# Optimization experiments

Measured on AMD Instinct MI355X. Metric: run time of the kernel, lower is better.

## Reference

```python
import jax, jax.numpy as jnp
import numpy as np

B, T, E, H = 16, 4096, 64, 8
K, GADD, RADD, REGION = 256, 8, 8, 64
MIN_SIGMA, SIGMA_SCALE, SIGMA_BOOST = 0.05, 1.0, 2.0
VS = K * (4 + GADD + RADD)


def setup_inputs() -> dict:
    key = jax.random.key(0)
    ks = jax.random.split(key, 10)
    return {
        "x": jax.random.normal(ks[0], (B, T, E), jnp.float32),
        "Wq": jax.random.normal(ks[1], (E, E * H), jnp.float32) / np.float32(np.sqrt(E)),
        "Wk": jax.random.normal(ks[2], (E, E * H), jnp.float32) / np.float32(np.sqrt(E)),
        "Wv": jax.random.normal(ks[3], (E, E * H), jnp.float32) / np.float32(np.sqrt(E)),
        "Wu": jax.random.normal(ks[4], (H * E, E), jnp.float32) / np.float32(np.sqrt(H * E)),
        "bu": jnp.zeros((E,), jnp.float32),
        "means_p": jax.random.normal(ks[5], (K, 2), jnp.float32),
        "sigmas_p": jax.random.normal(ks[6], (K,), jnp.float32),
        "global_ints": jax.random.randint(ks[7], (B, 1, K, GADD, 2), 0, T, jnp.int32),
        "local_offsets": jax.random.randint(ks[8], (B, 1, K, RADD, 2), 0, REGION, jnp.int32),
    }


def _flip(x):
    # util.flip: sort each (i, j) pair so row >= col (below-diagonal / causal)
    hi = jnp.max(x, axis=-1, keepdims=True)
    lo = jnp.min(x, axis=-1, keepdims=True)
    return jnp.concatenate([hi, lo], axis=-1)


def _forward(x, Wq, Wk, Wv, Wu, bu, means_p, sigmas_p, global_ints, local_offsets):
    b, t, e = x.shape
    h, k = H, K

    # ---- hyper(): continuous means/sigmas over the (t, t) attention matrix
    means = jnp.broadcast_to(means_p[None, None], (b, 1, k, 2))
    means = _flip(means)
    means = jax.nn.sigmoid(means) * (t - 1)                       # (b,1,k,2) in [0, t-1]
    sig = jax.nn.softplus(sigmas_p + SIGMA_BOOST) + MIN_SIGMA     # (k,)
    sigmas = jnp.broadcast_to((sig * t * SIGMA_SCALE)[None, None, :, None], (b, 1, k, 2))

    # ---- ngenerate: 2^rank floor/ceil neighbours + global + relative-window samples
    fl, ce = jnp.floor(means), jnp.ceil(means)
    pat = jnp.array([[0., 0.], [0., 1.], [1., 0.], [1., 1.]], jnp.float32)  # (4,2)
    neigh = fl[:, :, :, None, :] * (1.0 - pat) + ce[:, :, :, None, :] * pat
    neigh = jnp.clip(neigh, 0, t - 1).astype(jnp.int32)           # (b,1,k,4,2)
    lower = jnp.clip(jnp.floor(means) - REGION // 2, 0, t - REGION).astype(jnp.int32)
    local = lower[:, :, :, None, :] + local_offsets               # (b,1,k,RADD,2)
    idx = jnp.concatenate([neigh, global_ints, local], axis=3).reshape(b, 1, VS, 2)
    idx = _flip(idx)                                              # (b,1,VS,2), row >= col

    # ---- densities: unnormalized Gaussian weight of each int tuple under each point
    indfl = idx.astype(jnp.float32)
    diff = (indfl[:, :, :, None, :] - means[:, :, None, :, :]) / sigmas[:, :, None, :, :]
    props = jnp.exp(-0.5 * jnp.sum(diff * diff, axis=-1))         # (b,1,VS,K)

    # ---- nduplicates: zero all-but-one of identical index tuples per batch
    ids = idx[:, 0, :, 0] * t + idx[:, 0, :, 1]                   # (b, VS)
    def dupmask(v):
        o = jnp.argsort(v)
        s = v[o]
        d = jnp.concatenate([jnp.zeros((1,), bool), s[1:] == s[:-1]])
        return jnp.zeros((VS,), bool).at[o].set(d)
    dups = jax.vmap(dupmask)(ids)                                  # (b, VS)
    props = jnp.where(dups[:, None, :, None], 0.0, props)
    props = props / jnp.sum(props, axis=2, keepdims=True)
    weights = jnp.sum(props, axis=3)                               # mvalues == 1 -> (b,1,VS)

    # ---- Q/K/V projections, per-head dim = e
    scale = e ** -0.25
    q = (x @ Wq).reshape(b, t, h, e).transpose(0, 2, 1, 3).reshape(b * h, t, e) * scale
    kk = (x @ Wk).reshape(b, t, h, e).transpose(0, 2, 1, 3).reshape(b * h, t, e) * scale
    v = (x @ Wv).reshape(b, t, h, e).transpose(0, 2, 1, 3).reshape(b * h, t, e)

    rows = jnp.broadcast_to(idx[:, 0, None, :, 0], (b, h, VS)).reshape(b * h, VS)
    cols = jnp.broadcast_to(idx[:, 0, None, :, 1], (b, h, VS)).reshape(b * h, VS)
    w = jnp.broadcast_to(weights[:, 0, None, :], (b, h, VS)).reshape(b * h, VS)

    sq = jnp.take_along_axis(q, rows[:, :, None], axis=1)          # (b*h, VS, e)
    sk = jnp.take_along_axis(kk, cols[:, :, None], axis=1)
    dot = w * jnp.sum(sq * sk, axis=-1)                            # (b*h, VS)

    # ---- segment (row-wise) softmax over the sparse pattern
    seg = (jnp.arange(b * h, dtype=jnp.int32)[:, None] * t + rows).reshape(-1)
    dflat = dot.reshape(-1)
    m = jax.lax.stop_gradient(jax.ops.segment_max(dflat, seg, num_segments=b * h * t))
    ex = jnp.exp(dflat - m[seg])
    ssum = jax.ops.segment_sum(ex, seg, num_segments=b * h * t)
    p = ex / ssum[seg]                                             # (b*h*VS,)

    # ---- sparse batched matmul: scatter-add p * V[col] into rows
    gathered = jnp.take_along_axis(v, cols[:, :, None], axis=1).reshape(-1, e)
    out = jax.ops.segment_sum(p[:, None] * gathered, seg, num_segments=b * h * t)
    out = out.reshape(b, h, t, e).transpose(0, 2, 1, 3).reshape(b, t, h * e)
    return out @ Wu + bu


def reference(x, Wq, Wk, Wv, Wu, bu, means_p, sigmas_p, global_ints, local_offsets):
    return _forward(x, Wq, Wk, Wv, Wu, bu, means_p, sigmas_p, global_ints, local_offsets)
```

## Files before the change

### kernel.cpp

```cpp
#include <hip/hip_runtime.h>
#include <hip/hip_bf16.h>
#include <math.h>

#define B 16
#define T 4096
#define E 64
#define H 8
#define KP 256
#define GADD 8
#define RADD 8
#define REGION 64
#define VS (KP * (4 + GADD + RADD))
#define NH (H * E)
#define NCHUNK 20
#define HSZ 16384

typedef __attribute__((ext_vector_type(8))) short bf16x8;
typedef __attribute__((ext_vector_type(4))) float f32x4;

__device__ inline ushort f2bf(float f) {
    union { __hip_bfloat16 h; ushort u; } cv;
    cv.h = __float2bfloat16(f);
    return cv.u;
}
__device__ inline float bflo(uint32_t p) { return __uint_as_float(p << 16); }
__device__ inline float bfhi(uint32_t p) { return __uint_as_float(p & 0xffff0000u); }

__global__ void k_points(const float* __restrict__ means_p, const float* __restrict__ sigmas_p,
                         float* __restrict__ meansf, float* __restrict__ sigt) {
    int k = threadIdx.x;
    if (k >= KP) return;
    float a = means_p[2 * k], b = means_p[2 * k + 1];
    float hi = fmaxf(a, b), lo = fminf(a, b);
    meansf[2 * k]     = (1.f / (1.f + expf(-hi))) * (float)(T - 1);
    meansf[2 * k + 1] = (1.f / (1.f + expf(-lo))) * (float)(T - 1);
    float sp = sigmas_p[k] + 2.0f;
    float s = (sp > 20.f) ? sp : log1pf(expf(sp));
    sigt[k] = (s + 0.05f) * (float)T;
}

__global__ void k_wvu(const float* __restrict__ Wv, const float* __restrict__ Wu,
                      float* __restrict__ Wvu) {
    int idx = blockIdx.x * blockDim.x + threadIdx.x;
    if (idx >= E * NH) return;
    int i = idx / NH, c = idx % NH;
    int h = c / E, j = c % E;
    float acc = 0.f;
    for (int d = 0; d < E; ++d)
        acc += Wv[i * NH + h * E + d] * Wu[(h * E + d) * E + j];
    Wvu[i * NH + c] = acc;
}

__global__ void k_prep_x(const float* __restrict__ x, ushort* __restrict__ xb) {
    int i = (blockIdx.x * 256 + threadIdx.x) * 8;
    float4 a = *(const float4*)(x + i);
    float4 b = *(const float4*)(x + i + 4);
    uint4 r;
    r.x = (uint32_t)f2bf(a.x) | ((uint32_t)f2bf(a.y) << 16);
    r.y = (uint32_t)f2bf(a.z) | ((uint32_t)f2bf(a.w) << 16);
    r.z = (uint32_t)f2bf(b.x) | ((uint32_t)f2bf(b.y) << 16);
    r.w = (uint32_t)f2bf(b.z) | ((uint32_t)f2bf(b.w) << 16);
    *(uint4*)(xb + i) = r;
}

__global__ void k_prep_w(const float* __restrict__ Wq, const float* __restrict__ Wk,
                         const float* __restrict__ Wvu, ushort* __restrict__ wfrag) {
    int t = blockIdx.x * 256 + threadIdx.x;
    if (t >= 2 * 32 * 2 * 64) return;
    int lane = t & 63, kf = (t >> 6) & 1, nf = (t >> 7) & 31, z = t >> 12;
    int col = nf * 16 + (lane & 15);
    int krow = kf * 32 + (lane >> 4) * 8;
    uint32_t v[8];
    if (z == 0) {
        int h = col >> 6, d = col & 63;
        const float* wqrow = Wq + (size_t)d * NH + h * 64;
        #pragma unroll
        for (int j = 0; j < 8; ++j) {
            const float* wkrow = Wk + (size_t)(krow + j) * NH + h * 64;
            float acc = 0.f;
            for (int m = 0; m < 64; ++m) acc += wqrow[m] * wkrow[m];
            v[j] = f2bf(acc);
        }
    } else {
        #pragma unroll
        for (int j = 0; j < 8; ++j) v[j] = f2bf(Wvu[(size_t)(krow + j) * NH + col]);
    }
    uint4 r;
    r.x = v[0] | (v[1] << 16); r.y = v[2] | (v[3] << 16);
    r.z = v[4] | (v[5] << 16); r.w = v[6] | (v[7] << 16);
    *(uint4*)(wfrag + (size_t)t * 8) = r;
}

__global__ __launch_bounds__(256) void k_proj(const ushort* __restrict__ xb,
        const ushort* __restrict__ wfrag,
        __hip_bfloat16* __restrict__ xm, __hip_bfloat16* __restrict__ vu) {
    int z = blockIdx.y;
    __hip_bfloat16* outp = (z == 0) ? xm : vu;
    int row0 = blockIdx.x * 64;
    int wv = threadIdx.x >> 6, lane = threadIdx.x & 63;
    int arow = lane & 15, akoff = (lane >> 4) * 8;

    bf16x8 bfr[8][2];
    #pragma unroll
    for (int nf = 0; nf < 8; ++nf) {
        size_t base = ((size_t)((z * 32 + wv * 8 + nf) * 2) * 64 + lane) * 8;
        bfr[nf][0] = *(const bf16x8*)(wfrag + base);
        bfr[nf][1] = *(const bf16x8*)(wfrag + base + 64 * 8);
    }

    #pragma unroll
    for (int mf = 0; mf < 4; ++mf) {
        bf16x8 a0 = *(const bf16x8*)(xb + (size_t)(row0 + mf * 16 + arow) * 64 + akoff);
        bf16x8 a1 = *(const bf16x8*)(xb + (size_t)(row0 + mf * 16 + arow) * 64 + 32 + akoff);
        f32x4 acc[8];
        #pragma unroll
        for (int nf = 0; nf < 8; ++nf) {
            f32x4 t = {0.f, 0.f, 0.f, 0.f};
            t = __builtin_amdgcn_mfma_f32_16x16x32_bf16(a0, bfr[nf][0], t, 0, 0, 0);
            t = __builtin_amdgcn_mfma_f32_16x16x32_bf16(a1, bfr[nf][1], t, 0, 0, 0);
            acc[nf] = t;
        }
        int rbase = row0 + mf * 16 + (lane >> 4) * 4;
        #pragma unroll
        for (int rg = 0; rg < 4; ++rg) {
            uint4 o;
            o.x = (uint32_t)f2bf(acc[0][rg]) | ((uint32_t)f2bf(acc[1][rg]) << 16);
            o.y = (uint32_t)f2bf(acc[2][rg]) | ((uint32_t)f2bf(acc[3][rg]) << 16);
            o.z = (uint32_t)f2bf(acc[4][rg]) | ((uint32_t)f2bf(acc[5][rg]) << 16);
            o.w = (uint32_t)f2bf(acc[6][rg]) | ((uint32_t)f2bf(acc[7][rg]) << 16);
            *(uint4*)((ushort*)outp + (size_t)(rbase + rg) * NH + wv * 128 + (lane & 15) * 8) = o;
        }
    }
}

__global__ void k_build_idx(const int* __restrict__ g_ints, const int* __restrict__ l_offs,
                            const float* __restrict__ meansf,
                            int* __restrict__ idxrow, int* __restrict__ idxcol,
                            int* __restrict__ hkey, int* __restrict__ hval) {
    int b = blockIdx.y;
    int s = blockIdx.x * 256 + threadIdx.x;
    int* keys = hkey + b * HSZ;
    int* vals = hval + b * HSZ;
    int k = s / 20, slot = s % 20;
    float m0 = meansf[2 * k], m1 = meansf[2 * k + 1];
    int i0, i1;
    if (slot < 4) {
        float a  = (slot & 2) ? ceilf(m0) : floorf(m0);
        float bb = (slot & 1) ? ceilf(m1) : floorf(m1);
        a  = fminf(fmaxf(a, 0.f), (float)(T - 1));
        bb = fminf(fmaxf(bb, 0.f), (float)(T - 1));
        i0 = (int)a; i1 = (int)bb;
    } else if (slot < 12) {
        const int* p = g_ints + ((size_t)((b * KP + k) * GADD) + (slot - 4)) * 2;
        i0 = p[0]; i1 = p[1];
    } else {
        int lo0 = (int)fminf(fmaxf(floorf(m0) - (float)(REGION / 2), 0.f), (float)(T - REGION));
        int lo1 = (int)fminf(fmaxf(floorf(m1) - (float)(REGION / 2), 0.f), (float)(T - REGION));
        const int* p = l_offs + ((size_t)((b * KP + k) * RADD) + (slot - 12)) * 2;
        i0 = lo0 + p[0]; i1 = lo1 + p[1];
    }
    int row = max(i0, i1), col = min(i0, i1);
    idxrow[b * VS + s] = row;
    idxcol[b * VS + s] = col;
    int id = row * T + col;
    unsigned h = ((unsigned)id * 2654435761u) >> 18;
    while (true) {
        int old = atomicCAS(&keys[h], -1, id);
        if (old == -1 || old == id) { atomicMin(&vals[h], s); break; }
        h = (h + 1) & (HSZ - 1);
    }
}

__global__ __launch_bounds__(256) void k_local(const int* __restrict__ idxrow,
        const int* __restrict__ idxcol, const int* __restrict__ hkey,
        const int* __restrict__ hval, int* __restrict__ lrank, int* __restrict__ dup,
        int* __restrict__ chist) {
    int b = blockIdx.y, chunk = blockIdx.x;
    int tid = threadIdx.x;
    int s = chunk * 256 + tid;
    int r = idxrow[b * VS + s];
    int c = idxcol[b * VS + s];
    __shared__ int srow[256];
    srow[tid] = r;
    __syncthreads();
    int lr = 0;
    #pragma unroll 8
    for (int t = 0; t < 256; ++t) {
        int rt = srow[t];
        lr += (t < tid && rt == r);
    }
    lrank[b * VS + s] = lr;
    atomicAdd(&chist[(size_t)(b * T + r) * NCHUNK + chunk], 1);
    const int* keys = hkey + b * HSZ;
    const int* vals = hval + b * HSZ;
    int id = r * T + c;
    unsigned h = ((unsigned)id * 2654435761u) >> 18;
    while (keys[h] != id) h = (h + 1) & (HSZ - 1);
    dup[b * VS + s] = (vals[h] != s);
}

__global__ void k_chunkscan(int* __restrict__ chist, int* __restrict__ rowcnt) {
    int idx = blockIdx.x * 256 + threadIdx.x;
    int* p = chist + (size_t)idx * NCHUNK;
    int acc = 0;
    #pragma unroll
    for (int c = 0; c < NCHUNK; ++c) { int v = p[c]; p[c] = acc; acc += v; }
    rowcnt[idx] = acc;
}

__global__ void k_colsum(const int* __restrict__ idxrow, const int* __restrict__ idxcol,
                         const int* __restrict__ dup, const float* __restrict__ meansf,
                         const float* __restrict__ sigt, float* __restrict__ colsum) {
    int k = blockIdx.x, b = blockIdx.y;
    float m0 = meansf[2 * k], m1 = meansf[2 * k + 1];
    float inv = 1.f / sigt[k];
    float acc = 0.f;
    for (int s = threadIdx.x; s < VS; s += 256) {
        if (!dup[b * VS + s]) {
            float d0 = ((float)idxrow[b * VS + s] - m0) * inv;
            float d1 = ((float)idxcol[b * VS + s] - m1) * inv;
            acc += __expf(-0.5f * (d0 * d0 + d1 * d1));
        }
    }
    __shared__ float red[256];
    red[threadIdx.x] = acc;
    __syncthreads();
    for (int o = 128; o > 0; o >>= 1) {
        if (threadIdx.x < o) red[threadIdx.x] += red[threadIdx.x + o];
        __syncthreads();
    }
    if (threadIdx.x == 0) colsum[b * KP + k] = red[0];
}

__global__ void k_weights(const int* __restrict__ idxrow, const int* __restrict__ idxcol,
                          const int* __restrict__ dup, const float* __restrict__ meansf,
                          const float* __restrict__ sigt, const float* __restrict__ colsum,
                          float* __restrict__ wts) {
    int b = blockIdx.y;
    int s = blockIdx.x * 256 + threadIdx.x;
    __shared__ float sm[2 * KP], ss[KP], rc[KP];
    for (int k = threadIdx.x; k < KP; k += 256) {
        sm[2 * k] = meansf[2 * k];
        sm[2 * k + 1] = meansf[2 * k + 1];
        ss[k] = 1.f / sigt[k];
        rc[k] = 1.f / colsum[b * KP + k];
    }
    __syncthreads();
    float w = 0.f;
    if (!dup[b * VS + s]) {
        float r = (float)idxrow[b * VS + s], c = (float)idxcol[b * VS + s];
        #pragma unroll 4
        for (int k = 0; k < KP; ++k) {
            float d0 = (r - sm[2 * k]) * ss[k];
            float d1 = (c - sm[2 * k + 1]) * ss[k];
            w += __expf(-0.5f * (d0 * d0 + d1 * d1)) * rc[k];
        }
    }
    wts[b * VS + s] = w;
}

__global__ __launch_bounds__(1024) void k_scan(const int* __restrict__ rowcnt, int* __restrict__ rowptr) {
    int b = blockIdx.x, tid = threadIdx.x;
    __shared__ int part[1024];
    int v[4]; int loc = 0;
    for (int j = 0; j < 4; ++j) { v[j] = rowcnt[b * T + tid * 4 + j]; loc += v[j]; }
    part[tid] = loc;
    __syncthreads();
    for (int off = 1; off < 1024; off <<= 1) {
        int t = (tid >= off) ? part[tid - off] : 0;
        __syncthreads();
        part[tid] += t;
        __syncthreads();
    }
    int excl = part[tid] - loc;
    for (int j = 0; j < 4; ++j) { rowptr[b * (T + 1) + tid * 4 + j] = excl; excl += v[j]; }
    if (tid == 1023) rowptr[b * (T + 1) + T] = part[1023];
}

__global__ void k_scatter(const int* __restrict__ idxrow, const int* __restrict__ idxcol,
                          const float* __restrict__ wts, const int* __restrict__ lrank,
                          const int* __restrict__ chist, const int* __restrict__ rowptr,
                          int* __restrict__ scol, float* __restrict__ sw) {
    int b = blockIdx.y;
    int s = blockIdx.x * 256 + threadIdx.x;
    int r = idxrow[b * VS + s];
    int pos = rowptr[b * (T + 1) + r] + chist[(size_t)(b * T + r) * NCHUNK + (s >> 8)]
            + lrank[b * VS + s];
    scol[b * VS + pos] = idxcol[b * VS + s];
    sw[b * VS + pos] = wts[b * VS + s];
}

__global__ __launch_bounds__(256) void k_attn(
        const float* __restrict__ x, const __hip_bfloat16* __restrict__ xm,
        const __hip_bfloat16* __restrict__ vu, const int* __restrict__ rowptr,
        const int* __restrict__ scol, const float* __restrict__ sw,
        const float* __restrict__ bu, float* __restrict__ out) {
    int gr = blockIdx.x * 4 + (threadIdx.x >> 6);
    int b = gr >> 12;
    int r = gr & (T - 1);
    int lane = threadIdx.x & 63;
    int p0 = rowptr[b * (T + 1) + r], p1 = rowptr[b * (T + 1) + r + 1];

    const float* xrow = x + (size_t)gr * E + (lane & 15);
    float xv0 = xrow[0], xv1 = xrow[16], xv2 = xrow[32], xv3 = xrow[48];

    float m0 = -INFINITY, s0 = 0.f, m1 = -INFINITY, s1 = 0.f;
    float av[8] = {0.f,0.f,0.f,0.f,0.f,0.f,0.f,0.f};

    for (int e = p0; e < p1; ++e) {
        int c = scol[b * VS + e];
        float w = sw[b * VS + e];
        size_t off = ((size_t)(b * T + c)) * NH + lane * 8;
        uint4 k4 = *(const uint4*)((const ushort*)xm + off);
        float dp0 = xv0*bflo(k4.x) + xv1*bfhi(k4.x) + xv2*bflo(k4.y) + xv3*bfhi(k4.y);
        float dp1 = xv0*bflo(k4.z) + xv1*bfhi(k4.z) + xv2*bflo(k4.w) + xv3*bfhi(k4.w);
        dp0 += __shfl_xor(dp0, 1);
        dp0 += __shfl_xor(dp0, 2);
        dp0 += __shfl_xor(dp0, 4);
        dp0 += __shfl_xor(dp0, 8);
        dp1 += __shfl_xor(dp1, 1);
        dp1 += __shfl_xor(dp1, 2);
        dp1 += __shfl_xor(dp1, 4);
        dp1 += __shfl_xor(dp1, 8);
        float d0 = 0.125f * w * dp0;
        float d1 = 0.125f * w * dp1;
        uint4 v4 = *(const uint4*)((const ushort*)vu + off);
        float vf[8] = { bflo(v4.x), bfhi(v4.x), bflo(v4.y), bfhi(v4.y),
                        bflo(v4.z), bfhi(v4.z), bflo(v4.w), bfhi(v4.w) };
        float nm0 = fmaxf(m0, d0), c0 = __expf(m0 - nm0), t0 = __expf(d0 - nm0);
        float nm1 = fmaxf(m1, d1), c1 = __expf(m1 - nm1), t1 = __expf(d1 - nm1);
        s0 = s0 * c0 + t0; m0 = nm0;
        s1 = s1 * c1 + t1; m1 = nm1;
        #pragma unroll
        for (int u = 0; u < 4; ++u) av[u] = av[u] * c0 + t0 * vf[u];
        #pragma unroll
        for (int u = 4; u < 8; ++u) av[u] = av[u] * c1 + t1 * vf[u];
    }

    float i0 = (p1 > p0) ? (1.f / s0) : 0.f;
    float i1 = (p1 > p0) ? (1.f / s1) : 0.f;
    float res[4];
    #pragma unroll
    for (int u = 0; u < 4; ++u) {
        float v = av[u] * i0 + av[u + 4] * i1;
        v += __shfl_xor(v, 16);
        v += __shfl_xor(v, 32);
        res[u] = v;
    }
    if (lane < 16) {
        #pragma unroll
        for (int u = 0; u < 4; ++u)
            out[(size_t)gr * E + u * 16 + lane] = res[u] + bu[u * 16 + lane];
    }
}

extern "C" void kernel_launch(void* const* d_in, const int* in_sizes, int n_in,
                              void* d_out, int out_size, void* d_ws, size_t ws_size,
                              hipStream_t stream) {
    const float* x        = (const float*)d_in[0];
    const float* Wq       = (const float*)d_in[1];
    const float* Wk       = (const float*)d_in[2];
    const float* Wv       = (const float*)d_in[3];
    const float* Wu       = (const float*)d_in[4];
    const float* bu       = (const float*)d_in[5];
    const float* means_p  = (const float*)d_in[6];
    const float* sigmas_p = (const float*)d_in[7];
    const int*   g_ints   = (const int*)d_in[8];
    const int*   l_offs   = (const int*)d_in[9];
    float* out = (float*)d_out;

    char* ws = (char*)d_ws;
    size_t o = 0;
    auto alloc = [&](size_t bytes) -> void* {
        void* p = ws + o;
        o += (bytes + 255) & ~(size_t)255;
        return p;
    };
    __hip_bfloat16* xm  = (__hip_bfloat16*)alloc((size_t)B * T * NH * 2);
    __hip_bfloat16* vu  = (__hip_bfloat16*)alloc((size_t)B * T * NH * 2);
    ushort* xb    = (ushort*)alloc((size_t)B * T * E * 2);
    ushort* wfrag = (ushort*)alloc((size_t)2 * 32 * 2 * 64 * 8 * 2);
    float* Wvu    = (float*)alloc((size_t)E * NH * 4);
    float* meansf = (float*)alloc(KP * 2 * 4);
    float* sigt   = (float*)alloc(KP * 4);
    int*   idxrow = (int*)alloc((size_t)B * VS * 4);
    int*   idxcol = (int*)alloc((size_t)B * VS * 4);
    float* wts    = (float*)alloc((size_t)B * VS * 4);
    int*   lrank  = (int*)alloc((size_t)B * VS * 4);
    int*   dup    = (int*)alloc((size_t)B * VS * 4);
    float* colsum = (float*)alloc((size_t)B * KP * 4);
    int*   rowcnt = (int*)alloc((size_t)B * T * 4);
    int*   rowptr = (int*)alloc((size_t)B * (T + 1) * 4);
    int*   scol   = (int*)alloc((size_t)B * VS * 4);
    float* sw     = (float*)alloc((size_t)B * VS * 4);
    int*   hkey   = (int*)alloc((size_t)B * HSZ * 4);
    int*   hval   = (int*)alloc((size_t)B * HSZ * 4);
    int*   chist  = (int*)alloc((size_t)B * T * NCHUNK * 4);

    hipMemsetAsync(hkey, 0xFF, (size_t)B * HSZ * 4, stream);
    hipMemsetAsync(hval, 0x7F, (size_t)B * HSZ * 4, stream);
    hipMemsetAsync(chist, 0, (size_t)B * T * NCHUNK * 4, stream);

    k_points<<<1, 256, 0, stream>>>(means_p, sigmas_p, meansf, sigt);
    k_wvu<<<(E * NH + 255) / 256, 256, 0, stream>>>(Wv, Wu, Wvu);
    k_prep_x<<<(B * T * E / 8) / 256, 256, 0, stream>>>(x, xb);
    k_prep_w<<<(2 * 32 * 2 * 64 + 255) / 256, 256, 0, stream>>>(Wq, Wk, Wvu, wfrag);
    k_build_idx<<<dim3(VS / 256, B), 256, 0, stream>>>(g_ints, l_offs, meansf, idxrow, idxcol, hkey, hval);
    k_local<<<dim3(NCHUNK, B), 256, 0, stream>>>(idxrow, idxcol, hkey, hval, lrank, dup, chist);
    k_chunkscan<<<B * T / 256, 256, 0, stream>>>(chist, rowcnt);
    k_colsum<<<dim3(KP, B), 256, 0, stream>>>(idxrow, idxcol, dup, meansf, sigt, colsum);
    k_weights<<<dim3(VS / 256, B), 256, 0, stream>>>(idxrow, idxcol, dup, meansf, sigt, colsum, wts);
    k_scan<<<B, 1024, 0, stream>>>(rowcnt, rowptr);
    k_scatter<<<dim3(VS / 256, B), 256, 0, stream>>>(idxrow, idxcol, wts, lrank, chist, rowptr, scol, sw);
    k_proj<<<dim3(B * T / 64, 2), 256, 0, stream>>>(xb, wfrag, xm, vu);
    k_attn<<<B * T / 4, 256, 0, stream>>>(x, xm, vu, rowptr, scol, sw, bu, out);
}
```

Before: 188.8 us.

## Factor Gaussian weights into precomputed separable per-axis exp tables

Result: slower. 259.7 us (+37.5%).

```diff
diff --git a/kernel.cpp b/kernel.cpp
--- a/kernel.cpp
+++ b/kernel.cpp
@@ -14,6 +14,7 @@
 #define NH (H * E)
 #define NCHUNK 20
 #define HSZ 16384
+#define TK (T * KP)
 
 typedef __attribute__((ext_vector_type(8))) short bf16x8;
 typedef __attribute__((ext_vector_type(4))) float f32x4;
@@ -37,6 +38,30 @@
     float sp = sigmas_p[k] + 2.0f;
     float s = (sp > 20.f) ? sp : log1pf(expf(sp));
     sigt[k] = (s + 0.05f) * (float)T;
+}
+
+__global__ void k_tab_kt(const float* __restrict__ meansf, const float* __restrict__ sigt,
+                         float* __restrict__ ekt) {
+    int i = blockIdx.x * 256 + threadIdx.x;
+    int which = i >> 20;
+    int rem = i & (TK - 1);
+    int k = rem >> 12, t = rem & (T - 1);
+    float m = meansf[2 * k + which];
+    float inv = 1.f / sigt[k];
+    float d = ((float)t - m) * inv;
+    ekt[i] = __expf(-0.5f * d * d);
+}
+
+__global__ void k_tab_tk(const float* __restrict__ meansf, const float* __restrict__ sigt,
+                         float* __restrict__ etk) {
+    int i = blockIdx.x * 256 + threadIdx.x;
+    int which = i >> 20;
+    int rem = i & (TK - 1);
+    int t = rem >> 8, k = rem & (KP - 1);
+    float m = meansf[2 * k + which];
+    float inv = 1.f / sigt[k];
+    float d = ((float)t - m) * inv;
+    etk[i] = __expf(-0.5f * d * d);
 }
 
 __global__ void k_wvu(const float* __restrict__ Wv, const float* __restrict__ Wu,
@@ -209,18 +234,15 @@
 }
 
 __global__ void k_colsum(const int* __restrict__ idxrow, const int* __restrict__ idxcol,
-                         const int* __restrict__ dup, const float* __restrict__ meansf,
-                         const float* __restrict__ sigt, float* __restrict__ colsum) {
+                         const int* __restrict__ dup, const float* __restrict__ ekt,
+                         float* __restrict__ colsum) {
     int k = blockIdx.x, b = blockIdx.y;
-    float m0 = meansf[2 * k], m1 = meansf[2 * k + 1];
-    float inv = 1.f / sigt[k];
+    const float* e0 = ekt + (size_t)k * T;
+    const float* e1 = ekt + (size_t)TK + (size_t)k * T;
     float acc = 0.f;
     for (int s = threadIdx.x; s < VS; s += 256) {
-        if (!dup[b * VS + s]) {
-            float d0 = ((float)idxrow[b * VS + s] - m0) * inv;
-            float d1 = ((float)idxcol[b * VS + s] - m1) * inv;
-            acc += __expf(-0.5f * (d0 * d0 + d1 * d1));
-        }
+        if (!dup[b * VS + s])
+            acc += e0[idxrow[b * VS + s]] * e1[idxcol[b * VS + s]];
     }
     __shared__ float red[256];
     red[threadIdx.x] = acc;
@@ -233,28 +255,20 @@
 }
 
 __global__ void k_weights(const int* __restrict__ idxrow, const int* __restrict__ idxcol,
-                          const int* __restrict__ dup, const float* __restrict__ meansf,
-                          const float* __restrict__ sigt, const float* __restrict__ colsum,
-                          float* __restrict__ wts) {
+                          const int* __restrict__ dup, const float* __restrict__ etk,
+                          const float* __restrict__ colsum, float* __restrict__ wts) {
     int b = blockIdx.y;
     int s = blockIdx.x * 256 + threadIdx.x;
-    __shared__ float sm[2 * KP], ss[KP], rc[KP];
-    for (int k = threadIdx.x; k < KP; k += 256) {
-        sm[2 * k] = meansf[2 * k];
-        sm[2 * k + 1] = meansf[2 * k + 1];
-        ss[k] = 1.f / sigt[k];
-        rc[k] = 1.f / colsum[b * KP + k];
-    }
+    __shared__ float rc[KP];
+    rc[threadIdx.x] = 1.f / colsum[b * KP + threadIdx.x];
     __syncthreads();
     float w = 0.f;
     if (!dup[b * VS + s]) {
-        float r = (float)idxrow[b * VS + s], c = (float)idxcol[b * VS + s];
+        const float* er = etk + (size_t)idxrow[b * VS + s] * KP;
+        const float* ec = etk + (size_t)TK + (size_t)idxcol[b * VS + s] * KP;
         #pragma unroll 4
-        for (int k = 0; k < KP; ++k) {
-            float d0 = (r - sm[2 * k]) * ss[k];
-            float d1 = (c - sm[2 * k + 1]) * ss[k];
-            w += __expf(-0.5f * (d0 * d0 + d1 * d1)) * rc[k];
-        }
+        for (int k = 0; k < KP; ++k)
+            w += er[k] * ec[k] * rc[k];
     }
     wts[b * VS + s] = w;
 }
@@ -383,6 +397,8 @@
     float* Wvu    = (float*)alloc((size_t)E * NH * 4);
     float* meansf = (float*)alloc(KP * 2 * 4);
     float* sigt   = (float*)alloc(KP * 4);
+    float* ekt    = (float*)alloc((size_t)2 * TK * 4);
+    float* etk    = (float*)alloc((size_t)2 * TK * 4);
     int*   idxrow = (int*)alloc((size_t)B * VS * 4);
     int*   idxcol = (int*)alloc((size_t)B * VS * 4);
     float* wts    = (float*)alloc((size_t)B * VS * 4);
@@ -402,14 +418,16 @@
     hipMemsetAsync(chist, 0, (size_t)B * T * NCHUNK * 4, stream);
 
     k_points<<<1, 256, 0, stream>>>(means_p, sigmas_p, meansf, sigt);
+    k_tab_kt<<<2 * TK / 256, 256, 0, stream>>>(meansf, sigt, ekt);
+    k_tab_tk<<<2 * TK / 256, 256, 0, stream>>>(meansf, sigt, etk);
     k_wvu<<<(E * NH + 255) / 256, 256, 0, stream>>>(Wv, Wu, Wvu);
     k_prep_x<<<(B * T * E / 8) / 256, 256, 0, stream>>>(x, xb);
     k_prep_w<<<(2 * 32 * 2 * 64 + 255) / 256, 256, 0, stream>>>(Wq, Wk, Wvu, wfrag);
     k_build_idx<<<dim3(VS / 256, B), 256, 0, stream>>>(g_ints, l_offs, meansf, idxrow, idxcol, hkey, hval);
     k_local<<<dim3(NCHUNK, B), 256, 0, stream>>>(idxrow, idxcol, hkey, hval, lrank, dup, chist);
     k_chunkscan<<<B * T / 256, 256, 0, stream>>>(chist, rowcnt);
-    k_colsum<<<dim3(KP, B), 256, 0, stream>>>(idxrow, idxcol, dup, meansf, sigt, colsum);
-    k_weights<<<dim3(VS / 256, B), 256, 0, stream>>>(idxrow, idxcol, dup, meansf, sigt, colsum, wts);
+    k_colsum<<<dim3(KP, B), 256, 0, stream>>>(idxrow, idxcol, dup, ekt, colsum);
+    k_weights<<<dim3(VS / 256, B), 256, 0, stream>>>(idxrow, idxcol, dup, etk, colsum, wts);
     k_scan<<<B, 1024, 0, stream>>>(rowcnt, rowptr);
     k_scatter<<<dim3(VS / 256, B), 256, 0, stream>>>(idxrow, idxcol, wts, lrank, chist, rowptr, scol, sw);
     k_proj<<<dim3(B * T / 64, 2), 256, 0, stream>>>(xb, wfrag, xm, vu);
```
